# Performance work log

Measured on AMD Instinct MI355X. Metric: run time of the kernel, lower is better.

The kernel has to match this reference:

```python
import jax, jax.numpy as jnp
import numpy as np

N, E, F_IN, H, NSE, L, C, G = 50000, 800000, 128, 128, 16, 3, 10, 256


def setup_inputs() -> dict:
    key = jax.random.key(0)
    ks = jax.random.split(key, 32)
    sc = 0.05
    inp = {
        "x": jax.random.normal(ks[0], (N, F_IN), jnp.float32),
        "s": jax.random.normal(ks[1], (N, NSE), jnp.float32),
        "edge_index": jax.random.randint(ks[2], (2, E), 0, N, jnp.int64),
        "batch": jnp.sort(jax.random.randint(ks[3], (N,), 0, G, jnp.int64)),
        # pre: Linear(F_IN, H); embedding_s: Linear(NSE, H)
        "pre_w": jax.random.normal(ks[4], (F_IN, H), jnp.float32) * sc,
        "pre_b": jnp.zeros((H,), jnp.float32),
        "emb_w": jax.random.normal(ks[5], (NSE, H), jnp.float32) * sc,
        "emb_b": jnp.zeros((H,), jnp.float32),
        # per-layer GIN MLP: Linear(2H,H) -> ReLU -> Linear(H,H)
        "gin_w1": jax.random.normal(ks[6], (L, 2 * H, H), jnp.float32) * sc,
        "gin_b1": jnp.zeros((L, H), jnp.float32),
        "gin_w2": jax.random.normal(ks[7], (L, H, H), jnp.float32) * sc,
        "gin_b2": jnp.zeros((L, H), jnp.float32),
        # per-layer GCNConv(H, H)
        "gcn_w": jax.random.normal(ks[8], (L, H, H), jnp.float32) * sc,
        "gcn_b": jnp.zeros((L, H), jnp.float32),
        "whp_w": jax.random.normal(ks[9], (2 * H, H), jnp.float32) * sc,
        "whp_b": jnp.zeros((H,), jnp.float32),
        "post_w": jax.random.normal(ks[10], (H, H), jnp.float32) * sc,
        "post_b": jnp.zeros((H,), jnp.float32),
        "ro_w": jax.random.normal(ks[11], (H, C), jnp.float32) * sc,
        "ro_b": jnp.zeros((C,), jnp.float32),
    }
    return inp


def reference(x, s, edge_index, batch, pre_w, pre_b, emb_w, emb_b,
              gin_w1, gin_b1, gin_w2, gin_b2, gcn_w, gcn_b,
              whp_w, whp_b, post_w, post_b, ro_w, ro_b):
    src, dst = edge_index[0], edge_index[1]
    x = x @ pre_w + pre_b                      # [N, H]
    s = s @ emb_w + emb_b                      # [N, H]
    # GCN symmetric norm with self-loops (deg includes the +1 self loop)
    deg = jax.ops.segment_sum(jnp.ones((E,), x.dtype), dst, num_segments=N) + 1.0
    dinv = jax.lax.rsqrt(deg)                  # [N]
    enorm = (dinv[src] * dinv[dst])[:, None]   # [E, 1]
    self_norm = (dinv * dinv)[:, None]         # [N, 1]
    for i in range(L):
        xc = jnp.concatenate([x, s], axis=-1)  # [N, 2H]
        # GINConv (eps=0): nn(x_i + sum_j x_j)
        agg = jax.ops.segment_sum(xc[src], dst, num_segments=N)
        h = xc + agg
        h = jax.nn.relu(h @ gin_w1[i] + gin_b1[i]) @ gin_w2[i] + gin_b2[i]
        x = jax.nn.relu(h)                     # dropout is identity in eval mode
        # GCNConv on s stream
        hs = s @ gcn_w[i]
        sagg = jax.ops.segment_sum(hs[src] * enorm, dst, num_segments=N)
        s = jnp.tanh(sagg + hs * self_norm + gcn_b[i])
    x = jnp.concatenate([x, s], axis=-1) @ whp_w + whp_b
    g = jax.ops.segment_sum(x, batch, num_segments=G)   # global_add_pool [G, H]
    g = jax.nn.relu(g @ post_w + post_b)
    return jax.nn.log_softmax(g @ ro_w + ro_b, axis=1)
```

## Files before the change

kernel.cpp:

```cpp
#include <hip/hip_runtime.h>
#include <math.h>

typedef __attribute__((ext_vector_type(8))) short short8;
typedef __attribute__((ext_vector_type(4))) float f32x4;
typedef unsigned int uint;
typedef unsigned short ushort;

#define HGRID(n, b) (((n) + (b) - 1) / (b))

__device__ __forceinline__ ushort f2bu(float f) {
    uint x = __builtin_bit_cast(uint, f);
    x = (x + 0x7fffu + ((x >> 16) & 1u)) >> 16;
    return (ushort)x;
}
__device__ __forceinline__ float blo(uint u) {
    return __builtin_bit_cast(float, u << 16);
}
__device__ __forceinline__ float bhi(uint u) {
    return __builtin_bit_cast(float, u & 0xffff0000u);
}
__device__ __forceinline__ uint packbf(float a, float b) {
    return (uint)f2bu(a) | ((uint)f2bu(b) << 16);
}

__device__ __forceinline__ void gload16(const void* g, void* l) {
    __builtin_amdgcn_global_load_lds(
        (const __attribute__((address_space(1))) void*)g,
        (__attribute__((address_space(3))) void*)l, 16, 0, 0);
}


__global__ void count_kernel(const int* __restrict__ dst, int* __restrict__ cnt,
                             int* __restrict__ rank, int E) {
    int e = blockIdx.x * 256 + threadIdx.x;
    if (e < E) rank[e] = atomicAdd(&cnt[dst[e]], 1);
}

__global__ void scan_part(const int* __restrict__ cnt, int* __restrict__ bsum, int N) {
    __shared__ int sh[256];
    int b = blockIdx.x, t = threadIdx.x;
    int base = b * 1024 + t * 4;
    int tsum = 0;
    if (base + 3 < N) {
        int4 v = *(const int4*)(cnt + base);
        tsum = v.x + v.y + v.z + v.w;
    } else {
        #pragma unroll
        for (int k = 0; k < 4; ++k) if (base + k < N) tsum += cnt[base + k];
    }
    sh[t] = tsum;
    __syncthreads();
    for (int d = 128; d > 0; d >>= 1) {
        if (t < d) sh[t] += sh[t + d];
        __syncthreads();
    }
    if (t == 0) bsum[b] = sh[0];
}

__global__ void scan_fill(const int* __restrict__ cnt, const int* __restrict__ bsum,
                          int* __restrict__ offs, float* __restrict__ dinv,
                          int N, int E) {
    __shared__ int sh[256];
    __shared__ int sbase;
    int b = blockIdx.x, t = threadIdx.x;

    if (t < 64) {
        int s = 0;
        for (int i = t; i < b; i += 64) s += bsum[i];
        #pragma unroll
        for (int d = 32; d > 0; d >>= 1) s += __shfl_down(s, d, 64);
        if (t == 0) sbase = s;
    }

    int base = b * 1024 + t * 4;
    int c[4] = {0, 0, 0, 0};
    if (base + 3 < N) {
        int4 v = *(const int4*)(cnt + base);
        c[0] = v.x; c[1] = v.y; c[2] = v.z; c[3] = v.w;
    } else {
        #pragma unroll
        for (int k = 0; k < 4; ++k) if (base + k < N) c[k] = cnt[base + k];
    }
    int tsum = c[0] + c[1] + c[2] + c[3];
    sh[t] = tsum;
    __syncthreads();
    for (int d = 1; d < 256; d <<= 1) {
        int o = (t >= d) ? sh[t - d] : 0;
        __syncthreads();
        sh[t] += o;
        __syncthreads();
    }
    int run = sbase + sh[t] - tsum;
    #pragma unroll
    for (int k = 0; k < 4; ++k) {
        if (base + k < N) {
            offs[base + k] = run;
            dinv[base + k] = rsqrtf((float)c[k] + 1.0f);
            run += c[k];
        }
    }
    if (b == 0 && t == 0) offs[N] = E;
}

__global__ void fill_kernel(const int* __restrict__ src, const int* __restrict__ dst,
                            const int* __restrict__ offs, const int* __restrict__ rank,
                            const float* __restrict__ dinv, int2* __restrict__ epack, int E) {
    int e = blockIdx.x * 256 + threadIdx.x;
    if (e < E) {
        int d = dst[e];
        int sv = src[e];
        epack[offs[d] + rank[e]] = make_int2(sv * 64, __float_as_int(dinv[sv]));
    }
}


struct SetupArgs {
    const float *x, *s;
    const float *pre_w, *pre_b, *emb_w, *emb_b, *gin_w1, *gcn_w, *gin_w2;
    ushort *xs, *Wt_preemb, *Wt_dual, *Wt_gin2;
    float *bias_comb;
    int *cnt; float *gsum; int *cntg;
    int L, N, G;
};

__global__ void setup_kernel(SetupArgs a) {
    long idx = (long)blockIdx.x * 256 + threadIdx.x;
    long nconv = (long)a.N * 24;
    if (idx < nconv) {
        int n = (int)(idx / 24), ch = (int)(idx % 24);
        uint4 o = {0u, 0u, 0u, 0u};
        if (ch < 16) {
            const float4* px = (const float4*)(a.x + (long)n * 128 + ch * 8);
            float4 u = px[0], v = px[1];
            o.x = packbf(u.x, u.y); o.y = packbf(u.z, u.w);
            o.z = packbf(v.x, v.y); o.w = packbf(v.z, v.w);
        } else if (ch < 18) {
            const float4* ps = (const float4*)(a.s + (long)n * 16 + (ch - 16) * 8);
            float4 u = ps[0], v = ps[1];
            o.x = packbf(u.x, u.y); o.y = packbf(u.z, u.w);
            o.z = packbf(v.x, v.y); o.w = packbf(v.z, v.w);
        }
        *(uint4*)(a.xs + idx * 8) = o;
        return;
    }
    idx -= nconv;
    if (idx < 49152) {
        int c = (int)(idx / 192), k = (int)(idx % 192);
        float v = 0.f;
        if (c < 128) { if (k < 128) v = a.pre_w[(long)k * 128 + c]; }
        else if (k >= 128 && k < 144) v = a.emb_w[(long)(k - 128) * 128 + (c - 128)];
        a.Wt_preemb[idx] = f2bu(v);
        return;
    }
    idx -= 49152;
    if (idx < (long)a.L * 65536) {
        int i = (int)(idx / 65536);
        int r = (int)(idx % 65536);
        int c = r / 256, k = r % 256;
        float v = 0.f;
        if (c < 128) v = a.gin_w1[(long)i * 32768 + (long)k * 128 + c];
        else if (k >= 128) v = a.gcn_w[(long)i * 16384 + (long)(k - 128) * 128 + (c - 128)];
        a.Wt_dual[idx] = f2bu(v);
        return;
    }
    idx -= (long)a.L * 65536;
    if (idx < (long)a.L * 16384) {
        int i = (int)(idx / 16384);
        int r = (int)(idx % 16384);
        int c = r / 128, k = r % 128;
        a.Wt_gin2[idx] = f2bu(a.gin_w2[(long)i * 16384 + (long)k * 128 + c]);
        return;
    }
    idx -= (long)a.L * 16384;
    if (idx < 256) { a.bias_comb[idx] = (idx < 128) ? a.pre_b[idx] : a.emb_b[idx - 128]; return; }
    idx -= 256;
    if (idx < a.N) { a.cnt[idx] = 0; return; }
    idx -= a.N;
    if (idx < (long)a.G * 256) { a.gsum[idx] = 0.f; return; }
    idx -= (long)a.G * 256;
    if (idx < a.G) a.cntg[idx] = 0;
}


template<int KPAD, int BN>
__global__ __launch_bounds__(512) void lin_mfma(
    const ushort* __restrict__ A, int a_stride,
    const ushort* __restrict__ Wt, const float* __restrict__ bias,
    ushort* __restrict__ out, int o_stride, int N, int act, int interleaved)
{
    constexpr int BK = 64;
    constexpr int NF = BN / 64;
    __shared__ __align__(16) ushort LA[128][BK];
    __shared__ __align__(16) ushort LB[BN][BK];

    const int tid  = threadIdx.x;
    const int l    = tid & 63;
    const int w    = tid >> 6;
    const int wr   = w >> 2;
    const int wc   = w & 3;
    const int row0 = blockIdx.x * 128;
    const int l15  = l & 15;
    const int lhi  = l >> 4;
    const int lrow = l >> 3;
    const int lslot = l & 7;

    f32x4 acc[4][NF];
    #pragma unroll
    for (int m = 0; m < 4; ++m)
        #pragma unroll
        for (int n = 0; n < NF; ++n) acc[m][n] = (f32x4){0.f, 0.f, 0.f, 0.f};

    for (int k0 = 0; k0 < KPAD; k0 += BK) {
        __syncthreads();
        #pragma unroll
        for (int i = 0; i < 2; ++i) {
            int ci = w * 2 + i;
            int r  = ci * 8 + lrow;
            int gr = row0 + r; if (gr > N - 1) gr = N - 1;
            gload16(A + (long)gr * a_stride + k0 + ((lslot ^ (r & 7)) * 8), &LA[ci * 8][0]);
        }
        #pragma unroll
        for (int i = 0; i < NF; ++i) {
            int ci = w * NF + i;
            int c  = ci * 8 + lrow;
            gload16(Wt + (long)c * KPAD + k0 + ((lslot ^ (c & 7)) * 8), &LB[ci * 8][0]);
        }
        __syncthreads();
        #pragma unroll
        for (int kk = 0; kk < BK; kk += 32) {
            int chb = (kk >> 3) + lhi;
            short8 a[4];
            #pragma unroll
            for (int m = 0; m < 4; ++m) {
                int r = wr * 64 + m * 16 + l15;
                a[m] = *(const short8*)&LA[r][(chb ^ (r & 7)) * 8];
            }
            #pragma unroll
            for (int n = 0; n < NF; ++n) {
                int c = wc * (BN / 4) + n * 16 + l15;
                short8 b = *(const short8*)&LB[c][(chb ^ (c & 7)) * 8];
                #pragma unroll
                for (int m = 0; m < 4; ++m)
                    acc[m][n] = __builtin_amdgcn_mfma_f32_16x16x32_bf16(a[m], b, acc[m][n], 0, 0, 0);
            }
        }
    }

    #pragma unroll
    for (int n = 0; n < NF; ++n) {
        int col = wc * (BN / 4) + n * 16 + l15;
        float bv = bias ? bias[col] : 0.f;
        #pragma unroll
        for (int m = 0; m < 4; ++m) {
            #pragma unroll
            for (int j = 0; j < 4; ++j) {
                int gr = row0 + wr * 64 + m * 16 + (lhi << 2) + j;
                if (gr < N) {
                    float v = acc[m][n][j] + bv;
                    if (act) v = fmaxf(v, 0.f);
                    long off;
                    if (interleaved) {
                        int cc = col & 127;
                        off = (long)gr * 256 + 4 * (cc >> 1) + ((col >> 7) << 1) + (cc & 1);
                    } else {
                        off = (long)gr * o_stride + col;
                    }
                    out[off] = f2bu(v);
                }
            }
        }
    }
}


__global__ __launch_bounds__(512) void fused_g2d(
    const ushort* __restrict__ h1,
    const ushort* __restrict__ xcs,
    const ushort* __restrict__ Wg2,
    const float*  __restrict__ b2,
    const ushort* __restrict__ Wd,
    ushort* __restrict__ yh, int N)
{
    __shared__ __align__(16) ushort XT[128][128];
    __shared__ __align__(16) ushort SB[256][64];
    __shared__ __align__(16) ushort SA[128][64];

    const int tid  = threadIdx.x;
    const int l    = tid & 63;
    const int w    = tid >> 6;
    const int wr   = w >> 2;
    const int wc   = w & 3;
    const int row0 = blockIdx.x * 128;
    const int l15  = l & 15;
    const int lhi  = l >> 4;
    const int lrow = l >> 3;
    const int lslot = l & 7;

    f32x4 ax[4][2];
    #pragma unroll
    for (int m = 0; m < 4; ++m)
        #pragma unroll
        for (int n = 0; n < 2; ++n) ax[m][n] = (f32x4){0.f, 0.f, 0.f, 0.f};

    #pragma unroll
    for (int k0 = 0; k0 < 128; k0 += 64) {
        __syncthreads();
        #pragma unroll
        for (int i = 0; i < 2; ++i) {
            int ci = w * 2 + i;
            int r  = ci * 8 + lrow;
            int gr = row0 + r; if (gr > N - 1) gr = N - 1;
            gload16(h1 + (long)gr * 128 + k0 + ((lslot ^ (r & 7)) * 8), &SA[ci * 8][0]);
        }
        #pragma unroll
        for (int i = 0; i < 2; ++i) {
            int ci = w * 2 + i;
            int c  = ci * 8 + lrow;
            gload16(Wg2 + (long)c * 128 + k0 + ((lslot ^ (c & 7)) * 8), &SB[ci * 8][0]);
        }
        __syncthreads();
        #pragma unroll
        for (int kk = 0; kk < 64; kk += 32) {
            int chb = (kk >> 3) + lhi;
            short8 a[4];
            #pragma unroll
            for (int m = 0; m < 4; ++m) {
                int r = wr * 64 + m * 16 + l15;
                a[m] = *(const short8*)&SA[r][(chb ^ (r & 7)) * 8];
            }
            #pragma unroll
            for (int n = 0; n < 2; ++n) {
                int c = wc * 32 + n * 16 + l15;
                short8 b = *(const short8*)&SB[c][(chb ^ (c & 7)) * 8];
                #pragma unroll
                for (int m = 0; m < 4; ++m)
                    ax[m][n] = __builtin_amdgcn_mfma_f32_16x16x32_bf16(a[m], b, ax[m][n], 0, 0, 0);
            }
        }
    }
    #pragma unroll
    for (int n = 0; n < 2; ++n) {
        int col = wc * 32 + n * 16 + l15;
        float bv = b2[col];
        #pragma unroll
        for (int m = 0; m < 4; ++m) {
            #pragma unroll
            for (int j = 0; j < 4; ++j) {
                int row = wr * 64 + m * 16 + (lhi << 2) + j;
                float v = fmaxf(ax[m][n][j] + bv, 0.f);
                XT[row][(((col >> 3) ^ (row & 7)) << 3) + (col & 7)] = f2bu(v);
            }
        }
    }

    f32x4 ay[4][4];
    #pragma unroll
    for (int m = 0; m < 4; ++m)
        #pragma unroll
        for (int n = 0; n < 4; ++n) ay[m][n] = (f32x4){0.f, 0.f, 0.f, 0.f};

    #pragma unroll
    for (int k0 = 0; k0 < 256; k0 += 64) {
        __syncthreads();
        if (k0 >= 128) {
            #pragma unroll
            for (int i = 0; i < 2; ++i) {
                int ci = w * 2 + i;
                int r  = ci * 8 + lrow;
                int gr = row0 + r; if (gr > N - 1) gr = N - 1;
                gload16(xcs + (long)gr * 256 + 128 + (k0 - 128) + ((lslot ^ (r & 7)) * 8),
                        &SA[ci * 8][0]);
            }
        }
        #pragma unroll
        for (int i = 0; i < 4; ++i) {
            int ci = w * 4 + i;
            int c  = ci * 8 + lrow;
            gload16(Wd + (long)c * 256 + k0 + ((lslot ^ (c & 7)) * 8), &SB[ci * 8][0]);
        }
        __syncthreads();
        #pragma unroll
        for (int kk = 0; kk < 64; kk += 32) {
            short8 a[4];
            if (k0 < 128) {
                int chb = ((k0 + kk) >> 3) + lhi;
                #pragma unroll
                for (int m = 0; m < 4; ++m) {
                    int r = wr * 64 + m * 16 + l15;
                    a[m] = *(const short8*)&XT[r][(chb ^ (r & 7)) * 8];
                }
            } else {
                int chb = (kk >> 3) + lhi;
                #pragma unroll
                for (int m = 0; m < 4; ++m) {
                    int r = wr * 64 + m * 16 + l15;
                    a[m] = *(const short8*)&SA[r][(chb ^ (r & 7)) * 8];
                }
            }
            int chbb = (kk >> 3) + lhi;
            #pragma unroll
            for (int n = 0; n < 4; ++n) {
                int c = wc * 64 + n * 16 + l15;
                short8 b = *(const short8*)&SB[c][(chbb ^ (c & 7)) * 8];
                #pragma unroll
                for (int m = 0; m < 4; ++m)
                    ay[m][n] = __builtin_amdgcn_mfma_f32_16x16x32_bf16(a[m], b, ay[m][n], 0, 0, 0);
            }
        }
    }

    #pragma unroll
    for (int n = 0; n < 4; ++n) {
        int col = wc * 64 + n * 16 + l15;
        int cc = col & 127;
        #pragma unroll
        for (int m = 0; m < 4; ++m) {
            #pragma unroll
            for (int j = 0; j < 4; ++j) {
                int gr = row0 + wr * 64 + m * 16 + (lhi << 2) + j;
                if (gr < N) {
                    long off = (long)gr * 256 + 4 * (cc >> 1) + ((col >> 7) << 1) + (cc & 1);
                    yh[off] = f2bu(ay[m][n][j]);
                }
            }
        }
    }
}


__global__ __launch_bounds__(256) void fused_gather(
    const uint2* __restrict__ yh, const int* __restrict__ offs,
    const int2* __restrict__ epack,
    const float* __restrict__ dinv,
    const float* __restrict__ b1, const float* __restrict__ gb,
    uint* __restrict__ h1p, uint* __restrict__ xcp, int N)
{
    int node = blockIdx.x * 4 + (threadIdx.x >> 6);
    if (node >= N) return;
    node = __builtin_amdgcn_readfirstlane(node);
    int l = threadIdx.x & 63;

    uint2 self = yh[(long)node * 64 + l];
    float di = dinv[node];
    float g0 = blo(self.x), g1 = bhi(self.x);
    float s0 = 0.f, s1 = 0.f;

    int j0 = __builtin_amdgcn_readfirstlane(offs[node]);
    int j1 = __builtin_amdgcn_readfirstlane(offs[node + 1]);
    int jmid = j0 + ((j1 - j0) & ~15);

    for (int j = j0; j < jmid; j += 16) {
        int2 e[16]; uint2 v[16];
        #pragma unroll
        for (int k = 0; k < 16; ++k) e[k] = epack[j + k];
        #pragma unroll
        for (int k = 0; k < 16; ++k) v[k] = yh[e[k].x + l];
        #pragma unroll
        for (int k = 0; k < 16; ++k) {
            float ds = __int_as_float(e[k].y);
            g0 += blo(v[k].x);
            g1 += bhi(v[k].x);
            s0 += blo(v[k].y) * ds;
            s1 += bhi(v[k].y) * ds;
        }
    }
    for (int j = jmid; j < j1; j += 4) {
        int2 e[4]; uint2 v[4];
        #pragma unroll
        for (int k = 0; k < 4; ++k) {
            int jj = j + k;
            e[k] = epack[(jj < j1) ? jj : (j1 - 1)];
            if (jj >= j1) e[k].y = 0;
        }
        #pragma unroll
        for (int k = 0; k < 4; ++k) v[k] = yh[e[k].x + l];
        #pragma unroll
        for (int k = 0; k < 4; ++k) {
            float ds = __int_as_float(e[k].y);
            float m = (j + k < j1) ? 1.f : 0.f;
            g0 += blo(v[k].x) * m;
            g1 += bhi(v[k].x) * m;
            s0 += blo(v[k].y) * ds;
            s1 += bhi(v[k].y) * ds;
        }
    }

    float2 bb = ((const float2*)b1)[l];
    g0 = fmaxf(g0 + bb.x, 0.f);
    g1 = fmaxf(g1 + bb.y, 0.f);
    h1p[(long)node * 64 + l] = packbf(g0, g1);

    float dii = di * di;
    float2 gg = ((const float2*)gb)[l];
    float t0 = tanhf(s0 * di + blo(self.y) * dii + gg.x);
    float t1 = tanhf(s1 * di + bhi(self.y) * dii + gg.y);
    xcp[(long)node * 128 + 64 + l] = packbf(t0, t1);
}


__global__ void pool_kernel(const ushort* __restrict__ xc, const int* __restrict__ batch,
                            float* __restrict__ gsum, int* __restrict__ cntg, int N) {
    int c  = threadIdx.x;
    int n0 = blockIdx.x * 128;
    if (n0 >= N) return;
    int n1 = min(n0 + 128, N);
    int curg = batch[n0];
    float acc = 0.f;
    int cnt = 0;
    for (int n = n0; n < n1; ++n) {
        int b = batch[n];
        if (b != curg) {
            atomicAdd(&gsum[(long)curg * 256 + c], acc);
            if (c == 0) atomicAdd(&cntg[curg], cnt);
            acc = 0.f; cnt = 0;
            curg = b;
        }
        acc += blo((uint)xc[(long)n * 256 + c]);
        cnt++;
    }
    atomicAdd(&gsum[(long)curg * 256 + c], acc);
    if (c == 0) atomicAdd(&cntg[curg], cnt);
}


__global__ void head_kernel(const float* __restrict__ gsum, const int* __restrict__ cntg,
                            const float* __restrict__ whp_w, const float* __restrict__ whp_b,
                            const float* __restrict__ post_w, const float* __restrict__ post_b,
                            const float* __restrict__ ro_w, const float* __restrict__ ro_b,
                            float* __restrict__ out, int C) {
    __shared__ float row[256];
    __shared__ float xr[128];
    __shared__ float g2[128];
    __shared__ float lg[16];
    __shared__ float s_lse;
    int gi = blockIdx.x;
    int c  = threadIdx.x;
    row[c]       = gsum[(long)gi * 256 + c];
    row[c + 128] = gsum[(long)gi * 256 + 128 + c];
    __syncthreads();
    float cntf = (float)cntg[gi];
    float acc = cntf * whp_b[c];
    for (int k = 0; k < 256; ++k) acc += row[k] * whp_w[(long)k * 128 + c];
    xr[c] = acc;
    __syncthreads();
    float a2 = post_b[c];
    for (int k = 0; k < 128; ++k) a2 += xr[k] * post_w[k * 128 + c];
    g2[c] = fmaxf(a2, 0.f);
    __syncthreads();
    if (c < C) {
        float a = ro_b[c];
        for (int k = 0; k < 128; ++k) a += g2[k] * ro_w[k * C + c];
        lg[c] = a;
    }
    __syncthreads();
    if (c == 0) {
        float m = lg[0];
        for (int i = 1; i < C; ++i) m = fmaxf(m, lg[i]);
        float sum = 0.f;
        for (int i = 0; i < C; ++i) sum += expf(lg[i] - m);
        s_lse = m + logf(sum);
    }
    __syncthreads();
    if (c < C) out[(long)gi * C + c] = lg[c] - s_lse;
}


extern "C" void kernel_launch(void* const* d_in, const int* in_sizes, int n_in,
                              void* d_out, int out_size, void* d_ws, size_t ws_size,
                              hipStream_t stream) {
    const float* x      = (const float*)d_in[0];
    const float* s_in   = (const float*)d_in[1];
    const int*   ei     = (const int*)d_in[2];
    const int*   batch  = (const int*)d_in[3];
    const float* pre_w  = (const float*)d_in[4];
    const float* pre_b  = (const float*)d_in[5];
    const float* emb_w  = (const float*)d_in[6];
    const float* emb_b  = (const float*)d_in[7];
    const float* gin_w1 = (const float*)d_in[8];
    const float* gin_b1 = (const float*)d_in[9];
    const float* gin_w2 = (const float*)d_in[10];
    const float* gin_b2 = (const float*)d_in[11];
    const float* gcn_w  = (const float*)d_in[12];
    const float* gcn_b  = (const float*)d_in[13];
    const float* whp_w  = (const float*)d_in[14];
    const float* whp_b  = (const float*)d_in[15];
    const float* post_w = (const float*)d_in[16];
    const float* post_b = (const float*)d_in[17];
    const float* ro_w   = (const float*)d_in[18];
    const float* ro_b   = (const float*)d_in[19];

    const int H = 128;
    const int N = in_sizes[0] / 128;
    const int E = in_sizes[2] / 2;
    const int C = in_sizes[19];
    const int G = out_size / C;
    const int L = in_sizes[9] / H;

    const int* srcv = ei;
    const int* dstv = ei + E;

    char* p = (char*)d_ws;
    auto alloc = [&](size_t bytes) -> void* {
        void* r = (void*)p;
        p += (bytes + 255) & ~(size_t)255;
        return r;
    };
    ushort* xc   = (ushort*)alloc((size_t)N * 256 * 2);
    ushort* yh   = (ushort*)alloc((size_t)N * 256 * 2);
    ushort* h1   = (ushort*)alloc((size_t)N * 128 * 2);
    ushort* xs   = (ushort*)alloc((size_t)N * 192 * 2);
    ushort* Wt_preemb = (ushort*)alloc(256 * 192 * 2);
    ushort* Wt_dual   = (ushort*)alloc((size_t)L * 256 * 256 * 2);
    ushort* Wt_gin2   = (ushort*)alloc((size_t)L * 128 * 128 * 2);
    float*  bias_comb = (float*)alloc(256 * 4);
    float*  dinv = (float*)alloc((size_t)N * 4);
    float*  gsum = (float*)alloc((size_t)G * 256 * 4);
    int*    cntg = (int*)alloc((size_t)G * 4);
    int* cnt   = (int*)alloc((size_t)N * 4);
    int* offs  = (int*)alloc((size_t)(N + 1) * 4);
    int* rank  = (int*)alloc((size_t)E * 4);
    int* bsum  = (int*)alloc((size_t)HGRID(N, 1024) * 4);
    int2* epack = (int2*)alloc((size_t)E * 8);

    const int nb = HGRID(N, 1024);

    SetupArgs sa;
    sa.x = x; sa.s = s_in;
    sa.pre_w = pre_w; sa.pre_b = pre_b; sa.emb_w = emb_w; sa.emb_b = emb_b;
    sa.gin_w1 = gin_w1; sa.gcn_w = gcn_w; sa.gin_w2 = gin_w2;
    sa.xs = xs; sa.Wt_preemb = Wt_preemb; sa.Wt_dual = Wt_dual; sa.Wt_gin2 = Wt_gin2;
    sa.bias_comb = bias_comb; sa.cnt = cnt; sa.gsum = gsum; sa.cntg = cntg;
    sa.L = L; sa.N = N; sa.G = G;
    long setup_tot = (long)N * 24 + 49152 + (long)L * 65536 + (long)L * 16384 + 256
                   + N + (long)G * 256 + G;
    setup_kernel<<<HGRID(setup_tot, 256), 256, 0, stream>>>(sa);

    count_kernel<<<HGRID(E, 256), 256, 0, stream>>>(dstv, cnt, rank, E);
    scan_part<<<nb, 256, 0, stream>>>(cnt, bsum, N);
    scan_fill<<<nb, 256, 0, stream>>>(cnt, bsum, offs, dinv, N, E);
    fill_kernel<<<HGRID(E, 256), 256, 0, stream>>>(srcv, dstv, offs, rank, dinv, epack, E);

    const int lb = HGRID(N, 128);
    lin_mfma<192, 256><<<lb, 512, 0, stream>>>(xs, 192, Wt_preemb, bias_comb,
                                               xc, 256, N, 0, 0);
    lin_mfma<256, 256><<<lb, 512, 0, stream>>>(xc, 256, Wt_dual, nullptr, yh, 256, N, 0, 1);

    for (int i = 0; i < L; ++i) {
        fused_gather<<<HGRID(N, 4), 256, 0, stream>>>(
            (const uint2*)yh, offs, epack, dinv,
            gin_b1 + (size_t)i * H, gcn_b + (size_t)i * H,
            (uint*)h1, (uint*)xc, N);
        if (i < L - 1) {
            fused_g2d<<<lb, 512, 0, stream>>>(
                h1, xc, Wt_gin2 + (size_t)i * 16384, gin_b2 + (size_t)i * H,
                Wt_dual + (size_t)(i + 1) * 65536, yh, N);
        } else {
            lin_mfma<128, 128><<<lb, 512, 0, stream>>>(h1, 128, Wt_gin2 + (size_t)i * 16384,
                                                       gin_b2 + (size_t)i * H, xc, 256, N, 1, 0);
        }
    }

    pool_kernel<<<HGRID(N, 128), 256, 0, stream>>>(xc, batch, gsum, cntg, N);
    head_kernel<<<G, 128, 0, stream>>>(gsum, cntg, whp_w, whp_b,
                                       post_w, post_b, ro_w, ro_b, (float*)d_out, C);
}
```

Baseline: 377.8 us.

## Merge scan passes, fuse edge fill into pre-embedding GEMM, widen pool loads

The two-pass scan is replaced by a single scan kernel where each block re-sums every preceding count chunk itself to get its base offset. The CSR edge-pack fill is folded into the pre-embedding MFMA GEMM launch as extra blocks, so the two independent jobs run in one grid. The pool kernel now reads two bf16 values per thread with half the threads. These changes cut kernel launches and serialization points, at the cost of redundant prefix reads in the scan (quadratic in block count) and a mixed-role kernel whose GEMM blocks may run at lower occupancy.

```diff
diff --git a/kernel.cpp b/kernel.cpp
--- a/kernel.cpp
+++ b/kernel.cpp
@@ -36,40 +36,28 @@
     if (e < E) rank[e] = atomicAdd(&cnt[dst[e]], 1);
 }
 
-__global__ void scan_part(const int* __restrict__ cnt, int* __restrict__ bsum, int N) {
-    __shared__ int sh[256];
-    int b = blockIdx.x, t = threadIdx.x;
-    int base = b * 1024 + t * 4;
-    int tsum = 0;
-    if (base + 3 < N) {
-        int4 v = *(const int4*)(cnt + base);
-        tsum = v.x + v.y + v.z + v.w;
-    } else {
-        #pragma unroll
-        for (int k = 0; k < 4; ++k) if (base + k < N) tsum += cnt[base + k];
-    }
-    sh[t] = tsum;
-    __syncthreads();
-    for (int d = 128; d > 0; d >>= 1) {
-        if (t < d) sh[t] += sh[t + d];
-        __syncthreads();
-    }
-    if (t == 0) bsum[b] = sh[0];
-}
-
-__global__ void scan_fill(const int* __restrict__ cnt, const int* __restrict__ bsum,
-                          int* __restrict__ offs, float* __restrict__ dinv,
-                          int N, int E) {
+__global__ void scan_fill(const int* __restrict__ cnt, int* __restrict__ offs,
+                          float* __restrict__ dinv, int N, int E) {
     __shared__ int sh[256];
     __shared__ int sbase;
     int b = blockIdx.x, t = threadIdx.x;
 
-    if (t < 64) {
+    {
         int s = 0;
-        for (int i = t; i < b; i += 64) s += bsum[i];
-        #pragma unroll
-        for (int d = 32; d > 0; d >>= 1) s += __shfl_down(s, d, 64);
-        if (t == 0) sbase = s;
+        int pre4 = b * 256;
+        const int4* c4 = (const int4*)cnt;
+        for (int i = t; i < pre4; i += 256) {
+            int4 v = c4[i];
+            s += v.x + v.y + v.z + v.w;
+        }
+        sh[t] = s;
+        __syncthreads();
+        for (int d = 128; d > 0; d >>= 1) {
+            if (t < d) sh[t] += sh[t + d];
+            __syncthreads();
+        }
+        if (t == 0) sbase = sh[0];
+        __syncthreads();
     }
 
     int base = b * 1024 + t * 4;
@@ -100,17 +88,6 @@
         }
     }
     if (b == 0 && t == 0) offs[N] = E;
-}
-
-__global__ void fill_kernel(const int* __restrict__ src, const int* __restrict__ dst,
-                            const int* __restrict__ offs, const int* __restrict__ rank,
-                            const float* __restrict__ dinv, int2* __restrict__ epack, int E) {
-    int e = blockIdx.x * 256 + threadIdx.x;
-    if (e < E) {
-        int d = dst[e];
-        int sv = src[e];
-        epack[offs[d] + rank[e]] = make_int2(sv * 64, __float_as_int(dinv[sv]));
-    }
 }
 
 
@@ -183,7 +160,8 @@
 
 
 template<int KPAD, int BN>
-__global__ __launch_bounds__(512) void lin_mfma(
+__device__ __forceinline__ void lin_mfma_body(
+    int bid,
     const ushort* __restrict__ A, int a_stride,
     const ushort* __restrict__ Wt, const float* __restrict__ bias,
     ushort* __restrict__ out, int o_stride, int N, int act, int interleaved)
@@ -198,7 +176,7 @@
     const int w    = tid >> 6;
     const int wr   = w >> 2;
     const int wc   = w & 3;
-    const int row0 = blockIdx.x * 128;
+    const int row0 = bid * 128;
     const int l15  = l & 15;
     const int lhi  = l >> 4;
     const int lrow = l >> 3;
@@ -268,6 +246,35 @@
                     out[off] = f2bu(v);
                 }
             }
+        }
+    }
+}
+
+template<int KPAD, int BN>
+__global__ __launch_bounds__(512) void lin_mfma(
+    const ushort* __restrict__ A, int a_stride,
+    const ushort* __restrict__ Wt, const float* __restrict__ bias,
+    ushort* __restrict__ out, int o_stride, int N, int act, int interleaved)
+{
+    lin_mfma_body<KPAD, BN>(blockIdx.x, A, a_stride, Wt, bias, out, o_stride, N, act, interleaved);
+}
+
+
+__global__ __launch_bounds__(512) void preemb_fill(
+    const ushort* __restrict__ xs, const ushort* __restrict__ Wt_preemb,
+    const float* __restrict__ bias_comb, ushort* __restrict__ xc, int N, int PB,
+    const int* __restrict__ src, const int* __restrict__ dst,
+    const int* __restrict__ offs, const int* __restrict__ rank,
+    const float* __restrict__ dinv, int2* __restrict__ epack, int E)
+{
+    if ((int)blockIdx.x < PB) {
+        lin_mfma_body<192, 256>(blockIdx.x, xs, 192, Wt_preemb, bias_comb, xc, 256, N, 0, 0);
+    } else {
+        int e = (blockIdx.x - PB) * 512 + threadIdx.x;
+        if (e < E) {
+            int d = dst[e];
+            int sv = src[e];
+            epack[offs[d] + rank[e]] = make_int2(sv * 64, __float_as_int(dinv[sv]));
         }
     }
 }
@@ -505,20 +512,24 @@
     if (n0 >= N) return;
     int n1 = min(n0 + 128, N);
     int curg = batch[n0];
-    float acc = 0.f;
+    float a0 = 0.f, a1 = 0.f;
     int cnt = 0;
     for (int n = n0; n < n1; ++n) {
         int b = batch[n];
         if (b != curg) {
-            atomicAdd(&gsum[(long)curg * 256 + c], acc);
+            atomicAdd(&gsum[(long)curg * 256 + 2 * c], a0);
+            atomicAdd(&gsum[(long)curg * 256 + 2 * c + 1], a1);
             if (c == 0) atomicAdd(&cntg[curg], cnt);
-            acc = 0.f; cnt = 0;
+            a0 = a1 = 0.f; cnt = 0;
             curg = b;
         }
-        acc += blo((uint)xc[(long)n * 256 + c]);
+        uint v = *(const uint*)(xc + (long)n * 256 + 2 * c);
+        a0 += blo(v);
+        a1 += bhi(v);
         cnt++;
     }
-    atomicAdd(&gsum[(long)curg * 256 + c], acc);
+    atomicAdd(&gsum[(long)curg * 256 + 2 * c], a0);
+    atomicAdd(&gsum[(long)curg * 256 + 2 * c + 1], a1);
     if (c == 0) atomicAdd(&cntg[curg], cnt);
 }
 
@@ -619,7 +630,6 @@
     int* cnt   = (int*)alloc((size_t)N * 4);
     int* offs  = (int*)alloc((size_t)(N + 1) * 4);
     int* rank  = (int*)alloc((size_t)E * 4);
-    int* bsum  = (int*)alloc((size_t)HGRID(N, 1024) * 4);
     int2* epack = (int2*)alloc((size_t)E * 8);
 
     const int nb = HGRID(N, 1024);
@@ -636,13 +646,13 @@
     setup_kernel<<<HGRID(setup_tot, 256), 256, 0, stream>>>(sa);
 
     count_kernel<<<HGRID(E, 256), 256, 0, stream>>>(dstv, cnt, rank, E);
-    scan_part<<<nb, 256, 0, stream>>>(cnt, bsum, N);
-    scan_fill<<<nb, 256, 0, stream>>>(cnt, bsum, offs, dinv, N, E);
-    fill_kernel<<<HGRID(E, 256), 256, 0, stream>>>(srcv, dstv, offs, rank, dinv, epack, E);
+    scan_fill<<<nb, 256, 0, stream>>>(cnt, offs, dinv, N, E);
 
     const int lb = HGRID(N, 128);
-    lin_mfma<192, 256><<<lb, 512, 0, stream>>>(xs, 192, Wt_preemb, bias_comb,
-                                               xc, 256, N, 0, 0);
+    preemb_fill<<<lb + HGRID(E, 512), 512, 0, stream>>>(
+        xs, Wt_preemb, bias_comb, xc, N, lb,
+        srcv, dstv, offs, rank, dinv, epack, E);
+
     lin_mfma<256, 256><<<lb, 512, 0, stream>>>(xc, 256, Wt_dual, nullptr, yh, 256, N, 0, 1);
 
     for (int i = 0; i < L; ++i) {
@@ -660,7 +670,7 @@
         }
     }
 
-    pool_kernel<<<HGRID(N, 128), 256, 0, stream>>>(xc, batch, gsum, cntg, N);
+    pool_kernel<<<HGRID(N, 128), 128, 0, stream>>>(xc, batch, gsum, cntg, N);
     head_kernel<<<G, 128, 0, stream>>>(gsum, cntg, whp_w, whp_b,
                                        post_w, post_b, ro_w, ro_b, (float*)d_out, C);
 }
```

After: 380.2 us. Within noise of the previous version (+0.6%).
